# Optimization experiments

Hardware: AMD Instinct MI355X
Metric: run time of the kernel (lower is better)

The kernel has to match this reference:

```python
import jax, jax.numpy as jnp
import numpy as np

D_M, L_OBS, ALPHA, D_H, D_V, N_HEADS = 64, 256, 256, 256, 64, 8


def setup_inputs():
    key = jax.random.key(0)
    ks = jax.random.split(key, 18)
    x_ts = jax.random.normal(ks[0], (D_M, L_OBS), dtype=jnp.float32)
    t_raw = jax.random.uniform(ks[1], (D_M, L_OBS), dtype=jnp.float32) * ALPHA
    drop = jax.random.uniform(ks[2], (D_M, L_OBS)) < 0.5
    t_ts = jnp.where(drop, -1.0, t_raw)  # negative time == invalid observation
    global_means = jax.random.normal(ks[3], (D_M,), dtype=jnp.float32)
    s = 0.05
    return {
        'x_ts': x_ts, 't_ts': t_ts, 'global_means': global_means,
        'conv_w': jax.random.normal(ks[4], (D_H, D_M)) * s,
        'conv_b': jax.random.normal(ks[5], (D_H,)) * s,
        't2v_w': jax.random.normal(ks[6], (N_HEADS, D_V)),
        't2v_phi': jax.random.normal(ks[7], (N_HEADS, D_V)),
        'wq_w': jax.random.normal(ks[8], (N_HEADS, D_V, D_V)) * s,
        'wq_b': jax.random.normal(ks[9], (N_HEADS, D_V)) * s,
        'wk_w': jax.random.normal(ks[10], (N_HEADS, D_V, D_V)) * s,
        'wk_b': jax.random.normal(ks[11], (N_HEADS, D_V)) * s,
        'proj_w': jax.random.normal(ks[12], (D_H, N_HEADS)) * s,
        'proj_b': jax.random.normal(ks[13], (D_H,)) * s,
        'g1_w': jax.random.normal(ks[14], (D_H, 2 * D_H)) * s,
        'g1_b': jax.random.normal(ks[15], (D_H,)) * s,
        'g2_w': jax.random.normal(ks[16], (D_H, D_H)) * s,
        'g2_b': jax.random.normal(ks[17], (D_H,)) * s,
    }


def _time2vec(tau, w, phi):
    # tau [...], w/phi [H, D_V] -> [H, *tau.shape, D_V]; dim 0 linear, rest sin
    shp = (N_HEADS,) + (1,) * tau.ndim + (D_V,)
    full = w.reshape(shp) * tau[None, ..., None] + phi.reshape(shp)
    return jnp.concatenate([full[..., :1], jnp.sin(full[..., 1:])], axis=-1)


def _impute_row(x, t, gm):
    # ALPHA grid via int(time), then forward-fill starting from global mean.
    valid = (~jnp.isnan(x)) & (t >= 0)
    idx = t.astype(jnp.int32)  # truncation matches int(obs_time.item()) for t>=0
    inr = valid & (idx < ALPHA)
    seg = jnp.where(inr, idx, ALPHA)  # invalid obs go to dropped segment
    order = jnp.arange(L_OBS, dtype=jnp.int32)
    last = jax.ops.segment_max(jnp.where(inr, order, -1), seg,
                               num_segments=ALPHA + 1)[:ALPHA]
    present = last >= 0
    vals = x[jnp.clip(last, 0, L_OBS - 1)]          # value written to each slot
    pos = jnp.where(present, jnp.arange(ALPHA, dtype=jnp.int32), -1)
    lastpos = jax.lax.cummax(pos, axis=0)            # last observed slot <= t
    return jnp.where(lastpos >= 0, vals[jnp.clip(lastpos, 0, ALPHA - 1)], gm)


def _forward(x_ts, t_ts, global_means, conv_w, conv_b, t2v_w, t2v_phi,
             wq_w, wq_b, wk_w, wk_b, proj_w, proj_b, g1_w, g1_b, g2_w, g2_b):
    # --- imputation branch ---
    regular = jax.vmap(_impute_row)(x_ts, t_ts, global_means)  # [d_m, alpha]
    e_imp = (conv_w @ regular).T + conv_b                      # [alpha, d_h]
    # --- mTAND branch (masked attention over ragged observations) ---
    valid = (~jnp.isnan(x_ts)) & (t_ts >= 0)                   # [d_m, L]
    x_safe = jnp.where(valid, x_ts, 0.0)
    t_safe = jnp.where(valid, t_ts, 0.0)
    alpha_pts = jnp.arange(ALPHA, dtype=jnp.float32)
    theta_a = _time2vec(alpha_pts, t2v_w, t2v_phi)             # [H, alpha, d_v]
    q = jnp.einsum('had,hed->hae', theta_a, wq_w) + wq_b[:, None, :]
    theta_o = _time2vec(t_safe, t2v_w, t2v_phi)                # [H, d_m, L, d_v]
    k = jnp.einsum('hjld,hed->hjle', theta_o, wk_w) + wk_b[:, None, None, :]
    scores = jnp.einsum('hae,hjle->hjal', q, k) / np.float32(np.sqrt(D_V))
    scores = jnp.where(valid[None, :, None, :], scores, -1e9)  # exp underflows to 0
    attn = jax.nn.softmax(scores, axis=-1)                     # [H, d_m, alpha, L]
    # fully-invalid features: uniform attn * x_safe==0 -> zeros (matches torch)
    interp = jnp.einsum('hjal,jl->jah', attn, x_safe)          # [d_m, alpha, H]
    e_attn = (interp @ proj_w.T + proj_b).mean(axis=0)         # [alpha, d_h]
    # --- hidden_space gate ---
    concat = jnp.concatenate([e_imp, e_attn], axis=-1)         # [alpha, 2*d_h]
    g = jax.nn.sigmoid(jax.nn.relu(concat @ g1_w.T + g1_b) @ g2_w.T + g2_b)
    return g * e_imp + (1.0 - g) * e_attn                      # [alpha, d_h]


def reference(x_ts, t_ts, global_means, conv_w, conv_b, t2v_w, t2v_phi,
              wq_w, wq_b, wk_w, wk_b, proj_w, proj_b, g1_w, g1_b, g2_w, g2_b):
    return _forward(x_ts, t_ts, global_means, conv_w, conv_b, t2v_w, t2v_phi,
                    wq_w, wq_b, wk_w, wk_b, proj_w, proj_b, g1_w, g1_b, g2_w, g2_b)
```

## Files before the change

### kernel.cpp

```cpp
#include <hip/hip_runtime.h>

#define D_M     64
#define L_OBS   256
#define ALPHA   256
#define D_H     256
#define D_V     64
#define N_HEADS 8

typedef _Float16 half8 __attribute__((ext_vector_type(8)));
typedef float    f32x4 __attribute__((ext_vector_type(4)));

__global__ __launch_bounds__(256) void prep_kernel(
    const float* __restrict__ x_ts, const float* __restrict__ t_ts,
    const float* __restrict__ gm,
    const float* __restrict__ t2v_w, const float* __restrict__ t2v_phi,
    const float* __restrict__ wq_w, const float* __restrict__ wq_b,
    const float* __restrict__ wk_w,
    float* __restrict__ regular, float* __restrict__ QWbuf,
    float* __restrict__ QWabsG)
{
    const int tid = threadIdx.x;

    __shared__ int   last[ALPHA];
    __shared__ float vals[ALPHA];
    __shared__ int   wtot[4];
    __shared__ __align__(16) float wq_s[D_V][68];
    __shared__ __align__(16) float thA[16][68];
    __shared__ __align__(16) float QaT[16][68];

    if (blockIdx.x < D_M) {
        const int m  = blockIdx.x;
        const int l  = tid;
        const int wv = tid >> 6;
        const int ln = tid & 63;
        last[l] = -1;
        __syncthreads();
        float x = x_ts[m * L_OBS + l];
        float t = t_ts[m * L_OBS + l];
        bool valid = (x == x) && (t >= 0.0f);
        int idx = (int)t;
        if (valid && idx < ALPHA) atomicMax(&last[idx], l);
        __syncthreads();
        int li = last[l];
        vals[l] = (li >= 0) ? x_ts[m * L_OBS + li] : 0.0f;
        int p = (li >= 0) ? l : -1;
        #pragma unroll
        for (int s = 1; s < 64; s <<= 1) {
            int q = __shfl_up(p, s);
            if (ln >= s && q > p) p = q;
        }
        if (ln == 63) wtot[wv] = p;
        __syncthreads();
        int pre = -1;
        for (int w = 0; w < 4; w++)
            if (w < wv && wtot[w] > pre) pre = wtot[w];
        int lp = (pre > p) ? pre : p;
        regular[m * ALPHA + l] = (lp >= 0) ? vals[lp] : gm[m];
    } else {
        const int pb = blockIdx.x - D_M;
        const int h  = pb >> 4;
        const int a0 = (pb & 15) * 16;

        {
            const float4* w4 = (const float4*)(wq_w + h * D_V * D_V);
            #pragma unroll
            for (int i = 0; i < 4; i++) {
                int f = i * 256 + tid;
                float4 v = w4[f];
                int e = f >> 4, c = (f & 15) * 4;
                *(float4*)&wq_s[e][c] = v;
            }
        }
        {
            int al = tid >> 4, j0 = (tid & 15) * 4;
            float tv = (float)(a0 + al);
            #pragma unroll
            for (int j = 0; j < 4; j++) {
                int d = j0 + j;
                float f = t2v_w[h * D_V + d] * tv + t2v_phi[h * D_V + d];
                thA[al][d] = (d == 0) ? f : __sinf(f);
            }
        }
        __syncthreads();

        {
            const int e  = tid >> 2;
            const int ap = tid & 3;
            float accA[4] = {0.f, 0.f, 0.f, 0.f};
            const float4* wrow = (const float4*)&wq_s[e][0];
            #pragma unroll
            for (int j = 0; j < 16; j++) {
                float4 w = wrow[j];
                #pragma unroll
                for (int k = 0; k < 4; k++) {
                    float4 tv = *(const float4*)&thA[ap + 4 * k][j * 4];
                    accA[k] += w.x * tv.x + w.y * tv.y + w.z * tv.z + w.w * tv.w;
                }
            }
            float bq = wq_b[h * D_V + e];
            #pragma unroll
            for (int k = 0; k < 4; k++) QaT[ap + 4 * k][e] = accA[k] + bq;
        }
        __syncthreads();

        const int d  = tid >> 2;
        const int ap = tid & 3;
        float accB[4] = {0.f, 0.f, 0.f, 0.f};
        #pragma unroll 4
        for (int e4 = 0; e4 < 16; e4++) {
            const float* wkp = &wk_w[(h * D_V + e4 * 4) * D_V + d];
            float w0 = wkp[0];
            float w1 = wkp[D_V];
            float w2 = wkp[2 * D_V];
            float w3 = wkp[3 * D_V];
            #pragma unroll
            for (int k = 0; k < 4; k++) {
                float4 qv = *(const float4*)&QaT[ap + 4 * k][e4 * 4];
                accB[k] += qv.x * w0 + qv.y * w1 + qv.z * w2 + qv.w * w3;
            }
        }
        #pragma unroll
        for (int k = 0; k < 4; k++)
            QWbuf[h * D_V * ALPHA + d * ALPHA + a0 + ap + 4 * k] = accB[k];

        __syncthreads();
        #pragma unroll
        for (int k = 0; k < 4; k++)
            wq_s[d][ap + 4 * k] = (d == 0) ? 0.0f : fabsf(accB[k]);
        __syncthreads();
        if (tid < 16) {
            float s = 0.0f;
            #pragma unroll 8
            for (int dd = 0; dd < D_V; dd++) s += wq_s[dd][tid];
            QWabsG[h * ALPHA + a0 + tid] = s;
        }
    }
}

__global__ __launch_bounds__(256) void attn_mfma_kernel(
    const float* __restrict__ x_ts, const float* __restrict__ t_ts,
    const float* __restrict__ t2v_w, const float* __restrict__ t2v_phi,
    const float* __restrict__ QWbuf, const float* __restrict__ QWabsG,
    float* __restrict__ interp)
{
    const int ah  = blockIdx.x;
    const int m   = blockIdx.y;
    const int h   = blockIdx.z;
    const int tid = threadIdx.x;
    const int wv  = tid >> 6;
    const int ln  = tid & 63;
    const int lg  = ln >> 4;
    const int lc  = ln & 15;

    __shared__ float t_sh[L_OBS], x_sh[L_OBS], mk_sh[L_OBS];
    __shared__ float w_sh[D_V], phi_sh[D_V];
    __shared__ __align__(16) _Float16 hiB[2048];
    __shared__ __align__(16) _Float16 reB[2048];
    __shared__ float red_s[8];

    {
        float x = x_ts[m * L_OBS + tid];
        float t = t_ts[m * L_OBS + tid];
        bool v = (x == x) && (t >= 0.0f);
        x_sh[tid]  = v ? x : 0.0f;
        t_sh[tid]  = v ? t : 0.0f;
        mk_sh[tid] = v ? 0.0f : -1.0e9f;
        float tmx = v ? t : -3.0e38f;
        float tmn = v ? t : 3.0e38f;
        #pragma unroll
        for (int s = 1; s < 64; s <<= 1) {
            tmx = fmaxf(tmx, __shfl_xor(tmx, s));
            tmn = fminf(tmn, __shfl_xor(tmn, s));
        }
        if (ln == 0) { red_s[wv] = tmx; red_s[4 + wv] = tmn; }
    }
    if (tid < D_V)          w_sh[tid]         = t2v_w[h * D_V + tid];
    else if (tid < 2 * D_V) phi_sh[tid - D_V] = t2v_phi[h * D_V + tid - D_V];
    __syncthreads();

    const float tmaxv = fmaxf(fmaxf(red_s[0], red_s[1]), fmaxf(red_s[2], red_s[3]));
    const float tminv = fminf(fminf(red_s[4], red_s[5]), fminf(red_s[6], red_s[7]));
    const bool  anyv  = tmaxv > -1.0e37f;

    const float* __restrict__ QWh = QWbuf + h * D_V * ALPHA;
    const float w0 = w_sh[0], p0 = phi_sh[0];
    const float SCALE2 = 0.18033688011112042f;

    half8 ahf[2][2], arf[2][2];
    float qw0[2][4], c0b[2][4];
    #pragma unroll
    for (int at = 0; at < 2; at++) {
        const int abase = ah * 128 + wv * 32 + at * 16;
        const int arowA = abase + lc;
        #pragma unroll
        for (int kb = 0; kb < 2; kb++) {
            #pragma unroll
            for (int j = 0; j < 8; j++) {
                int d = 1 + kb * 32 + ((j >> 2) << 4) + (lg << 2) + (j & 3);
                float q = (d < D_V) ? QWh[d * ALPHA + arowA] : 0.0f;
                _Float16 qh = (_Float16)q;
                ahf[at][kb][j] = qh;
                arf[at][kb][j] = (_Float16)(q - (float)qh);
            }
        }
        const int arowD = abase + lg * 4;
        #pragma unroll
        for (int r = 0; r < 4; r++) {
            float q0 = QWh[arowD + r];
            qw0[at][r] = q0;
            float u = q0 * w0;
            float lin = q0 * p0 + fmaxf(u * tmaxv, u * tminv);
            c0b[at][r] = -(lin + QWabsG[h * ALPHA + arowD + r]);
        }
    }

    float ssum[2][4], axs[2][4];
    #pragma unroll
    for (int at = 0; at < 2; at++)
        #pragma unroll
        for (int r = 0; r < 4; r++) { ssum[at][r] = 0.0f; axs[at][r] = 0.0f; }

    const int wc  = tid >> 5;
    const int lcw = (tid >> 1) & 15;
    const int dB  = 1 + (wc >> 2) * 32 + (wc & 3) * 4 + ((tid & 1) << 4);

    auto write_frags = [&](int lt, int buf) {
        float tvw = t_sh[lt * 16 + lcw];
        float s0 = __sinf(fmaf(w_sh[(dB + 0) & 63], tvw, phi_sh[(dB + 0) & 63]));
        float s1 = __sinf(fmaf(w_sh[(dB + 1) & 63], tvw, phi_sh[(dB + 1) & 63]));
        float s2 = __sinf(fmaf(w_sh[(dB + 2) & 63], tvw, phi_sh[(dB + 2) & 63]));
        float s3 = __sinf(fmaf(w_sh[(dB + 3) & 63], tvw, phi_sh[(dB + 3) & 63]));
        union { _Float16 hv[4]; float2 f2; } hw, rw;
        hw.hv[0] = (_Float16)s0; hw.hv[1] = (_Float16)s1;
        hw.hv[2] = (_Float16)s2; hw.hv[3] = (_Float16)s3;
        rw.hv[0] = (_Float16)(s0 - (float)hw.hv[0]);
        rw.hv[1] = (_Float16)(s1 - (float)hw.hv[1]);
        rw.hv[2] = (_Float16)(s2 - (float)hw.hv[2]);
        rw.hv[3] = (_Float16)(s3 - (float)hw.hv[3]);
        *(float2*)&hiB[buf * 1024 + tid * 4] = hw.f2;
        *(float2*)&reB[buf * 1024 + tid * 4] = rw.f2;
    };

    write_frags(0, 0);
    __syncthreads();

    for (int lt = 0; lt < 16; lt++) {
        const int cur = lt & 1;
        half8 bh[2], br[2];
        #pragma unroll
        for (int kb = 0; kb < 2; kb++) {
            int fi = cur * 1024 + ((kb * 4 + lg) * 16 + lc) * 8;
            bh[kb] = *(const half8*)&hiB[fi];
            br[kb] = *(const half8*)&reB[fi];
        }
        if (lt < 15) write_frags(lt + 1, cur ^ 1);

        const int l = lt * 16 + lc;
        const float tv  = t_sh[l];
        const float xv  = x_sh[l];
        const float mkv = mk_sh[l];
        const float tau = fmaf(w0, tv, p0);

        #pragma unroll
        for (int at = 0; at < 2; at++) {
            f32x4 acc;
            #pragma unroll
            for (int r = 0; r < 4; r++)
                acc[r] = fmaf(qw0[at][r], tau, c0b[at][r]);
            #pragma unroll
            for (int kb = 0; kb < 2; kb++) {
                acc = __builtin_amdgcn_mfma_f32_16x16x32_f16(ahf[at][kb], bh[kb], acc, 0, 0, 0);
                acc = __builtin_amdgcn_mfma_f32_16x16x32_f16(ahf[at][kb], br[kb], acc, 0, 0, 0);
                acc = __builtin_amdgcn_mfma_f32_16x16x32_f16(arf[at][kb], bh[kb], acc, 0, 0, 0);
            }
            #pragma unroll
            for (int r = 0; r < 4; r++) {
                float p = __builtin_amdgcn_exp2f(fmaf(acc[r], SCALE2, mkv));
                ssum[at][r] += p;
                axs[at][r]   = fmaf(p, xv, axs[at][r]);
            }
        }
        __syncthreads();
    }

    #pragma unroll
    for (int at = 0; at < 2; at++) {
        #pragma unroll
        for (int r = 0; r < 4; r++) {
            float S = ssum[at][r];
            float A = axs[at][r];
            S += __shfl_xor(S, 1); A += __shfl_xor(A, 1);
            S += __shfl_xor(S, 2); A += __shfl_xor(A, 2);
            S += __shfl_xor(S, 4); A += __shfl_xor(A, 4);
            S += __shfl_xor(S, 8); A += __shfl_xor(A, 8);
            if (lc == 0) {
                int a = ah * 128 + wv * 32 + at * 16 + lg * 4 + r;
                interp[a * (D_M * N_HEADS) + m * N_HEADS + h] =
                    anyv ? (A / S) : 0.0f;
            }
        }
    }
}

__global__ __launch_bounds__(256) void final_kernel(
    const float* __restrict__ regular, const float* __restrict__ interp,
    const float* __restrict__ conv_w, const float* __restrict__ conv_b,
    const float* __restrict__ proj_w, const float* __restrict__ proj_b,
    const float* __restrict__ g1_w, const float* __restrict__ g1_b,
    const float* __restrict__ g2_w, const float* __restrict__ g2_b,
    float* __restrict__ out)
{
    const int a = blockIdx.x;
    const int tid = threadIdx.x;
    __shared__ float isum_s[N_HEADS];
    __shared__ __align__(16) float col[D_M];
    __shared__ __align__(16) float c_s[2 * D_H];
    __shared__ __align__(16) float h_s[D_H];

    if (tid < 64) {
        const float4* i4 = (const float4*)&interp[a * (D_M * N_HEADS) + tid * 8];
        float4 v0 = i4[0], v1 = i4[1];
        float v[8] = {v0.x, v0.y, v0.z, v0.w, v1.x, v1.y, v1.z, v1.w};
        #pragma unroll
        for (int s = 1; s < 64; s <<= 1) {
            #pragma unroll
            for (int j = 0; j < 8; j++) v[j] += __shfl_xor(v[j], s);
        }
        if (tid == 0) {
            #pragma unroll
            for (int j = 0; j < 8; j++) isum_s[j] = v[j];
        }
    } else if (tid < 128) {
        col[tid - 64] = regular[(tid - 64) * ALPHA + a];
    }
    __syncthreads();

    float vattn;
    {
        const float4* p4 = (const float4*)&proj_w[tid * N_HEADS];
        float4 v0 = p4[0], v1 = p4[1];
        float sum = v0.x * isum_s[0] + v0.y * isum_s[1] + v0.z * isum_s[2]
                  + v0.w * isum_s[3] + v1.x * isum_s[4] + v1.y * isum_s[5]
                  + v1.z * isum_s[6] + v1.w * isum_s[7];
        vattn = proj_b[tid] + sum * (1.0f / 64.0f);
    }
    float vimp;
    {
        const float4* row = (const float4*)&conv_w[tid * D_M];
        const float4* c4  = (const float4*)col;
        float s0 = 0.f, s1 = 0.f, s2 = 0.f, s3 = 0.f;
        #pragma unroll
        for (int i = 0; i < D_M / 4; i++) {
            float4 r = row[i]; float4 c = c4[i];
            s0 += r.x * c.x; s1 += r.y * c.y; s2 += r.z * c.z; s3 += r.w * c.w;
        }
        vimp = conv_b[tid] + ((s0 + s1) + (s2 + s3));
    }
    c_s[tid]       = vimp;
    c_s[D_H + tid] = vattn;
    __syncthreads();

    {
        const float4* grow = (const float4*)&g1_w[tid * 2 * D_H];
        const float4* c4 = (const float4*)c_s;
        float s0 = 0.f, s1 = 0.f, s2 = 0.f, s3 = 0.f;
        #pragma unroll 8
        for (int i = 0; i < (2 * D_H) / 4; i++) {
            float4 g = grow[i]; float4 c = c4[i];
            s0 += g.x * c.x; s1 += g.y * c.y; s2 += g.z * c.z; s3 += g.w * c.w;
        }
        float hid = g1_b[tid] + ((s0 + s1) + (s2 + s3));
        h_s[tid] = fmaxf(hid, 0.0f);
    }
    __syncthreads();
    {
        const float4* grow = (const float4*)&g2_w[tid * D_H];
        const float4* h4 = (const float4*)h_s;
        float s0 = 0.f, s1 = 0.f, s2 = 0.f, s3 = 0.f;
        #pragma unroll 8
        for (int i = 0; i < D_H / 4; i++) {
            float4 g = grow[i]; float4 hh = h4[i];
            s0 += g.x * hh.x; s1 += g.y * hh.y; s2 += g.z * hh.z; s3 += g.w * hh.w;
        }
        float z = g2_b[tid] + ((s0 + s1) + (s2 + s3));
        float gate = 1.0f / (1.0f + __expf(-z));
        out[a * D_H + tid] = gate * vimp + (1.0f - gate) * vattn;
    }
}

extern "C" void kernel_launch(void* const* d_in, const int* in_sizes, int n_in,
                              void* d_out, int out_size, void* d_ws, size_t ws_size,
                              hipStream_t stream)
{
    (void)in_sizes; (void)n_in; (void)out_size; (void)ws_size;

    const float* x_ts    = (const float*)d_in[0];
    const float* t_ts    = (const float*)d_in[1];
    const float* gm      = (const float*)d_in[2];
    const float* conv_w  = (const float*)d_in[3];
    const float* conv_b  = (const float*)d_in[4];
    const float* t2v_w   = (const float*)d_in[5];
    const float* t2v_phi = (const float*)d_in[6];
    const float* wq_w    = (const float*)d_in[7];
    const float* wq_b    = (const float*)d_in[8];
    const float* wk_w    = (const float*)d_in[9];
    const float* proj_w  = (const float*)d_in[11];
    const float* proj_b  = (const float*)d_in[12];
    const float* g1_w    = (const float*)d_in[13];
    const float* g1_b    = (const float*)d_in[14];
    const float* g2_w    = (const float*)d_in[15];
    const float* g2_b    = (const float*)d_in[16];

    float* out = (float*)d_out;

    float* ws      = (float*)d_ws;
    float* regular = ws;
    float* QWbuf   = regular + D_M * ALPHA;
    float* interp  = QWbuf + N_HEADS * D_V * ALPHA;
    float* QWabs   = interp + ALPHA * D_M * N_HEADS;

    prep_kernel<<<D_M + 128, 256, 0, stream>>>(
        x_ts, t_ts, gm, t2v_w, t2v_phi, wq_w, wq_b, wk_w,
        regular, QWbuf, QWabs);
    attn_mfma_kernel<<<dim3(2, D_M, N_HEADS), 256, 0, stream>>>(
        x_ts, t_ts, t2v_w, t2v_phi, QWbuf, QWabs, interp);
    final_kernel<<<ALPHA, 256, 0, stream>>>(
        regular, interp, conv_w, conv_b, proj_w, proj_b,
        g1_w, g1_b, g2_w, g2_b, out);
}
```

Measured before the change: 57.59 us.

## Compact valid observations and process two L-tiles per barrier in attention

Uses a ballot and popcount to stream-compact the valid (x, t) observations into shared memory, so the attention loop only iterates over ceil(Lv/16) tiles instead of all 16. With roughly half the observations dropped, this removes about half of the MFMA, sin and exp work. Fragment buffers are enlarged so each barrier-separated stage covers two 16-wide tiles, halving the number of __syncthreads. The padding mask is now derived from the compacted count. The cost is extra shared memory and some data-dependent loop bounds.

```diff
diff --git a/kernel.cpp b/kernel.cpp
--- a/kernel.cpp
+++ b/kernel.cpp
@@ -152,19 +152,21 @@
     const int lg  = ln >> 4;
     const int lc  = ln & 15;
 
-    __shared__ float t_sh[L_OBS], x_sh[L_OBS], mk_sh[L_OBS];
+    __shared__ float xc[L_OBS], tc[L_OBS];
     __shared__ float w_sh[D_V], phi_sh[D_V];
-    __shared__ __align__(16) _Float16 hiB[2048];
-    __shared__ __align__(16) _Float16 reB[2048];
+    __shared__ __align__(16) _Float16 hiB[2][2048];
+    __shared__ __align__(16) _Float16 reB[2][2048];
     __shared__ float red_s[8];
-
-    {
-        float x = x_ts[m * L_OBS + tid];
-        float t = t_ts[m * L_OBS + tid];
-        bool v = (x == x) && (t >= 0.0f);
-        x_sh[tid]  = v ? x : 0.0f;
-        t_sh[tid]  = v ? t : 0.0f;
-        mk_sh[tid] = v ? 0.0f : -1.0e9f;
+    __shared__ int   cnt_s[4];
+
+    xc[tid] = 0.0f;
+    tc[tid] = 0.0f;
+    float x = x_ts[m * L_OBS + tid];
+    float t = t_ts[m * L_OBS + tid];
+    bool  v = (x == x) && (t >= 0.0f);
+    unsigned long long bal = __ballot(v);
+    if (ln == 0) cnt_s[wv] = __popcll(bal);
+    {
         float tmx = v ? t : -3.0e38f;
         float tmn = v ? t : 3.0e38f;
         #pragma unroll
@@ -177,6 +179,14 @@
     if (tid < D_V)          w_sh[tid]         = t2v_w[h * D_V + tid];
     else if (tid < 2 * D_V) phi_sh[tid - D_V] = t2v_phi[h * D_V + tid - D_V];
     __syncthreads();
+
+    const int c0 = cnt_s[0], c1 = cnt_s[1], c2 = cnt_s[2], c3 = cnt_s[3];
+    const int Lv = c0 + c1 + c2 + c3;
+    {
+        int base = (wv > 0 ? c0 : 0) + (wv > 1 ? c1 : 0) + (wv > 2 ? c2 : 0);
+        unsigned long long lm = (1ull << ln) - 1ull;
+        if (v) { int p = base + __popcll(bal & lm); xc[p] = x; tc[p] = t; }
+    }
 
     const float tmaxv = fmaxf(fmaxf(red_s[0], red_s[1]), fmaxf(red_s[2], red_s[3]));
     const float tminv = fminf(fminf(red_s[4], red_s[5]), fminf(red_s[6], red_s[7]));
@@ -224,8 +234,8 @@
     const int lcw = (tid >> 1) & 15;
     const int dB  = 1 + (wc >> 2) * 32 + (wc & 3) * 4 + ((tid & 1) << 4);
 
-    auto write_frags = [&](int lt, int buf) {
-        float tvw = t_sh[lt * 16 + lcw];
+    auto write_frags = [&](int lt, int buf, int slot) {
+        float tvw = tc[lt * 16 + lcw];
         float s0 = __sinf(fmaf(w_sh[(dB + 0) & 63], tvw, phi_sh[(dB + 0) & 63]));
         float s1 = __sinf(fmaf(w_sh[(dB + 1) & 63], tvw, phi_sh[(dB + 1) & 63]));
         float s2 = __sinf(fmaf(w_sh[(dB + 2) & 63], tvw, phi_sh[(dB + 2) & 63]));
@@ -237,47 +247,59 @@
         rw.hv[1] = (_Float16)(s1 - (float)hw.hv[1]);
         rw.hv[2] = (_Float16)(s2 - (float)hw.hv[2]);
         rw.hv[3] = (_Float16)(s3 - (float)hw.hv[3]);
-        *(float2*)&hiB[buf * 1024 + tid * 4] = hw.f2;
-        *(float2*)&reB[buf * 1024 + tid * 4] = rw.f2;
+        *(float2*)&hiB[buf][slot * 1024 + tid * 4] = hw.f2;
+        *(float2*)&reB[buf][slot * 1024 + tid * 4] = rw.f2;
     };
 
-    write_frags(0, 0);
-    __syncthreads();
-
-    for (int lt = 0; lt < 16; lt++) {
-        const int cur = lt & 1;
-        half8 bh[2], br[2];
-        #pragma unroll
-        for (int kb = 0; kb < 2; kb++) {
-            int fi = cur * 1024 + ((kb * 4 + lg) * 16 + lc) * 8;
-            bh[kb] = *(const half8*)&hiB[fi];
-            br[kb] = *(const half8*)&reB[fi];
-        }
-        if (lt < 15) write_frags(lt + 1, cur ^ 1);
-
-        const int l = lt * 16 + lc;
-        const float tv  = t_sh[l];
-        const float xv  = x_sh[l];
-        const float mkv = mk_sh[l];
-        const float tau = fmaf(w0, tv, p0);
-
-        #pragma unroll
-        for (int at = 0; at < 2; at++) {
-            f32x4 acc;
-            #pragma unroll
-            for (int r = 0; r < 4; r++)
-                acc[r] = fmaf(qw0[at][r], tau, c0b[at][r]);
+    const int nst  = (Lv + 15) >> 4;
+    const int nreg = (nst + 1) >> 1;
+
+    __syncthreads();
+    write_frags(0, 0, 0);
+    write_frags(1, 0, 1);
+    __syncthreads();
+
+    for (int rg = 0; rg < nreg; rg++) {
+        const int cur = rg & 1;
+        if (rg + 1 < nreg) {
+            write_frags(2 * rg + 2, cur ^ 1, 0);
+            write_frags(2 * rg + 3, cur ^ 1, 1);
+        }
+        #pragma unroll
+        for (int s = 0; s < 2; s++) {
+            const int st = 2 * rg + s;
+            if (st >= nst) break;
+            half8 bh[2], br[2];
             #pragma unroll
             for (int kb = 0; kb < 2; kb++) {
-                acc = __builtin_amdgcn_mfma_f32_16x16x32_f16(ahf[at][kb], bh[kb], acc, 0, 0, 0);
-                acc = __builtin_amdgcn_mfma_f32_16x16x32_f16(ahf[at][kb], br[kb], acc, 0, 0, 0);
-                acc = __builtin_amdgcn_mfma_f32_16x16x32_f16(arf[at][kb], bh[kb], acc, 0, 0, 0);
-            }
-            #pragma unroll
-            for (int r = 0; r < 4; r++) {
-                float p = __builtin_amdgcn_exp2f(fmaf(acc[r], SCALE2, mkv));
-                ssum[at][r] += p;
-                axs[at][r]   = fmaf(p, xv, axs[at][r]);
+                int fi = s * 1024 + ((kb * 4 + lg) * 16 + lc) * 8;
+                bh[kb] = *(const half8*)&hiB[cur][fi];
+                br[kb] = *(const half8*)&reB[cur][fi];
+            }
+            const int l = st * 16 + lc;
+            const float tv  = tc[l];
+            const float xv  = xc[l];
+            const float mkv = (l < Lv) ? 0.0f : -1.0e9f;
+            const float tau = fmaf(w0, tv, p0);
+
+            #pragma unroll
+            for (int at = 0; at < 2; at++) {
+                f32x4 acc;
+                #pragma unroll
+                for (int r = 0; r < 4; r++)
+                    acc[r] = fmaf(qw0[at][r], tau, c0b[at][r]);
+                #pragma unroll
+                for (int kb = 0; kb < 2; kb++) {
+                    acc = __builtin_amdgcn_mfma_f32_16x16x32_f16(ahf[at][kb], bh[kb], acc, 0, 0, 0);
+                    acc = __builtin_amdgcn_mfma_f32_16x16x32_f16(ahf[at][kb], br[kb], acc, 0, 0, 0);
+                    acc = __builtin_amdgcn_mfma_f32_16x16x32_f16(arf[at][kb], bh[kb], acc, 0, 0, 0);
+                }
+                #pragma unroll
+                for (int r = 0; r < 4; r++) {
+                    float p = __builtin_amdgcn_exp2f(fmaf(acc[r], SCALE2, mkv));
+                    ssum[at][r] += p;
+                    axs[at][r]   = fmaf(p, xv, axs[at][r]);
+                }
             }
         }
         __syncthreads();
```

Result: faster. 52.72 us (-8.5%).
